# Kernel tuning notes

Hardware: AMD Instinct MI355X
Metric: run time of the kernel (lower is better)

## Reference

```python
import jax, jax.numpy as jnp
import numpy as np

N = 50000      # nodes (cells)
E = 800000     # directed edges
IN, H1, H2, Z = 512, 128, 128, 64


def setup_inputs() -> dict:
    key = jax.random.key(0)
    ks = jax.random.split(key, 12)
    x = jax.random.normal(ks[0], (N, IN), jnp.float32)
    edge_index = jax.random.randint(ks[1], (2, E), 0, N, dtype=jnp.int64)

    def glorot(k, i, o):
        return jax.random.normal(k, (i, o), jnp.float32) * np.float32(1.0 / np.sqrt(i))

    return {
        "x": x,
        "edge_index": edge_index,
        "W1": glorot(ks[2], IN, H1), "b1": jnp.zeros((H1,), jnp.float32),
        "W2": glorot(ks[3], H1, H2), "b2": jnp.zeros((H2,), jnp.float32),
        "Wm": glorot(ks[4], H2, Z),  "bm": jnp.zeros((Z,), jnp.float32),
        "Ws": glorot(ks[5], H2, Z),  "bs": jnp.zeros((Z,), jnp.float32),
    }


def _gcn_norm(edge_index, n):
    # PyG GCNConv default: add self-loops, sym-normalize D^-1/2 (A+I) D^-1/2
    loops = jnp.arange(n, dtype=edge_index.dtype)
    src = jnp.concatenate([edge_index[0], loops])
    dst = jnp.concatenate([edge_index[1], loops])
    deg = jax.ops.segment_sum(jnp.ones_like(dst, jnp.float32), dst, num_segments=n)
    dis = jnp.where(deg > 0, jax.lax.rsqrt(jnp.maximum(deg, 1.0)), 0.0)
    norm = dis[src] * dis[dst]  # [E+N]
    return src, dst, norm


def _gcn_conv(x, W, b, src, dst, norm, n):
    h = x @ W                          # [N, out] transform first
    msg = h[src] * norm[:, None]       # gather + scale
    out = jax.ops.segment_sum(msg, dst, num_segments=n)  # scatter-add at targets
    return out + b


def reference(x, edge_index, W1, b1, W2, b2, Wm, bm, Ws, bs):
    n = x.shape[0]
    src, dst, norm = _gcn_norm(edge_index, n)
    h = jax.nn.relu(_gcn_conv(x, W1, b1, src, dst, norm, n))
    h = jax.nn.relu(_gcn_conv(h, W2, b2, src, dst, norm, n))
    # dropout p=0.4 is identity in eval mode
    z_mean = _gcn_conv(h, Wm, bm, src, dst, norm, n)
    z_log_std = _gcn_conv(h, Ws, bs, src, dst, norm, n)
    return (z_mean, z_log_std)
```

## Files before the change

kernel.cpp:

```cpp
#include <hip/hip_runtime.h>


using u16 = unsigned short;
typedef __attribute__((ext_vector_type(8))) short short8;
typedef __attribute__((ext_vector_type(4))) float f32x4;

__device__ __forceinline__ void split_bf16(float f, u16& hi, u16& lo) {
    unsigned b = __float_as_uint(f);
    hi = (u16)(b >> 16);
    float rem = f - __uint_as_float(b & 0xFFFF0000u);
    lo = (u16)(__float_as_uint(rem) >> 16);
}

__device__ __forceinline__ int block_mode(const int* __restrict__ ew, int* sflag) {
    if (threadIdx.x == 0) *sflag = 0;
    __syncthreads();
    if (ew[2 * (int)threadIdx.x + 1] != 0) atomicOr(sflag, 1);
    __syncthreads();
    return *sflag ? 0 : 1;
}

__global__ void deg_kernel(const int* __restrict__ ew, int* __restrict__ deg, int E) {
    __shared__ int sflag;
    int mode = block_mode(ew, &sflag);
    int e = blockIdx.x * blockDim.x + threadIdx.x;
    if (e >= E) return;
    int d = mode ? ew[2 * E + 2 * e] : ew[E + e];
    atomicAdd(&deg[d], 1);
}

__global__ void scan_block_kernel(const int* __restrict__ deg, int* __restrict__ rowptr,
                                  int* __restrict__ aux, float* __restrict__ dis, int N) {
    __shared__ int s[256];
    int i = blockIdx.x * 256 + threadIdx.x;
    int v = (i < N) ? deg[i] : 0;
    if (i < N) dis[i] = rsqrtf((float)v + 1.0f);
    s[threadIdx.x] = v;
    __syncthreads();
    for (int off = 1; off < 256; off <<= 1) {
        int t = (threadIdx.x >= off) ? s[threadIdx.x - off] : 0;
        __syncthreads();
        s[threadIdx.x] += t;
        __syncthreads();
    }
    if (i < N) rowptr[i] = s[threadIdx.x] - v;
    if (threadIdx.x == 255) aux[blockIdx.x] = s[255];
}

__global__ void scan_aux_kernel(int* __restrict__ aux, int nb) {
    __shared__ int s[256];
    int i = threadIdx.x;
    int v = (i < nb) ? aux[i] : 0;
    s[i] = v;
    __syncthreads();
    for (int off = 1; off < 256; off <<= 1) {
        int t = (i >= off) ? s[i - off] : 0;
        __syncthreads();
        s[i] += t;
        __syncthreads();
    }
    if (i < nb) aux[i] = s[i] - v;
}

__global__ void add_offsets_kernel(int* __restrict__ rowptr, const int* __restrict__ aux,
                                   int N, int E) {
    int i = blockIdx.x * 256 + threadIdx.x;
    if (i < N) rowptr[i] += aux[i >> 8];
    if (i == 0) rowptr[N] = E;
}

__global__ void fill_csr_kernel(const int* __restrict__ ew,
                                const int* __restrict__ rowptr, int* __restrict__ cursor,
                                int* __restrict__ csr_src, int E) {
    __shared__ int sflag;
    int mode = block_mode(ew, &sflag);
    int e = blockIdx.x * blockDim.x + threadIdx.x;
    if (e >= E) return;
    int s = mode ? ew[2 * e] : ew[e];
    int d = mode ? ew[2 * E + 2 * e] : ew[E + e];
    int pos = rowptr[d] + atomicAdd(&cursor[d], 1);
    csr_src[pos] = s;
}

__global__ void conv_all_kernel(const float* __restrict__ W1, const float* __restrict__ W2,
                                const float* __restrict__ Wm, const float* __restrict__ Ws,
                                u16* __restrict__ B1h, u16* __restrict__ B1l,
                                u16* __restrict__ B2h, u16* __restrict__ B2l,
                                u16* __restrict__ Bch, u16* __restrict__ Bcl) {
    int idx = blockIdx.x * 256 + threadIdx.x;
    u16 h, l;
    if (idx < 65536) {
        int t = idx >> 13;
        int ks = (idx >> 9) & 15;
        int L = (idx >> 3) & 63;
        int q = idx & 7;
        int col = t * 16 + (L & 15);
        int k = ks * 32 + (L >> 4) * 8 + q;
        split_bf16(W1[k * 128 + col], h, l);
        B1h[idx] = h;
        B1l[idx] = l;
    } else if (idx < 81920) {
        int o = idx - 65536;
        int t = o >> 11;
        int ks = (o >> 9) & 3;
        int L = (o >> 3) & 63;
        int q = o & 7;
        int col = t * 16 + (L & 15);
        int k = ks * 32 + (L >> 4) * 8 + q;
        split_bf16(W2[k * 128 + col], h, l);
        B2h[o] = h;
        B2l[o] = l;
    } else if (idx < 98304) {
        int o = idx - 81920;
        int t = o >> 11;
        int ks = (o >> 9) & 3;
        int L = (o >> 3) & 63;
        int q = o & 7;
        int col = t * 16 + (L & 15);
        int k = ks * 32 + (L >> 4) * 8 + q;
        float f = (col < 64) ? Wm[k * 64 + col] : Ws[k * 64 + (col - 64)];
        split_bf16(f, h, l);
        Bch[o] = h;
        Bcl[o] = l;
    }
}

#define TILE_OFF(t) ((t) * 520)

__global__ __launch_bounds__(256) void gemm_mfma(const float* __restrict__ A,
                                                 const u16* __restrict__ Bfh,
                                                 const u16* __restrict__ Bfl,
                                                 float* __restrict__ C,
                                                 int N, int K) {
    __shared__ __align__(16) u16 AsH[4 * 520], AsL[4 * 520];

    const int tid = threadIdx.x;
    const int w = tid >> 6, lane = tid & 63;
    const int m16 = lane & 15, quad = lane >> 4;
    const int row0 = blockIdx.x * 64;

    const int s_ar = w * 16 + (lane & 15);
    const int s_ak = (lane >> 4) * 8;
    const int a_dst = TILE_OFF(w) + lane * 8;

    const int R = (w >> 1) * 32, Cc = (w & 1) * 64;
    const int atile = (w >> 1) * 2;
    const int btile = (w & 1) * 4;

    const int ksteps = K >> 5;
    const u16* bfh = Bfh + ((size_t)btile * ksteps) * 512 + lane * 8;
    const u16* bfl = Bfl + ((size_t)btile * ksteps) * 512 + lane * 8;

    f32x4 acc[2][4];
#pragma unroll
    for (int i = 0; i < 2; ++i)
#pragma unroll
        for (int j = 0; j < 4; ++j) acc[i][j] = (f32x4)0.f;

    const int grow = row0 + s_ar;
    const bool ok = (grow < N);
    const float* aptr = A + (size_t)grow * K + s_ak;

    float av[8];
    {
        f32x4 v0 = (f32x4)0.f, v1 = (f32x4)0.f;
        if (ok) { v0 = *(const f32x4*)&aptr[0]; v1 = *(const f32x4*)&aptr[4]; }
#pragma unroll
        for (int q = 0; q < 4; ++q) { av[q] = v0[q]; av[4 + q] = v1[q]; }
    }

    for (int ks = 0; ks < ksteps; ++ks) {
        short8 fbh[4], fbl[4];
#pragma unroll
        for (int j = 0; j < 4; ++j) {
            fbh[j] = *(const short8*)(bfh + (size_t)(j * ksteps + ks) * 512);
            fbl[j] = *(const short8*)(bfl + (size_t)(j * ksteps + ks) * 512);
        }

        short8 ah, al;
#pragma unroll
        for (int q = 0; q < 8; ++q) {
            u16 h, l;
            split_bf16(av[q], h, l);
            ah[q] = (short)h;
            al[q] = (short)l;
        }
        __syncthreads();
        *(short8*)&AsH[a_dst] = ah;
        *(short8*)&AsL[a_dst] = al;
        __syncthreads();

        if (ks + 1 < ksteps) {
            const int k0 = (ks + 1) * 32;
            f32x4 v0 = (f32x4)0.f, v1 = (f32x4)0.f;
            if (ok) { v0 = *(const f32x4*)&aptr[k0]; v1 = *(const f32x4*)&aptr[k0 + 4]; }
#pragma unroll
            for (int q = 0; q < 4; ++q) { av[q] = v0[q]; av[4 + q] = v1[q]; }
        }

        short8 fah[2], fal[2];
#pragma unroll
        for (int i = 0; i < 2; ++i) {
            fah[i] = *(const short8*)&AsH[TILE_OFF(atile + i) + lane * 8];
            fal[i] = *(const short8*)&AsL[TILE_OFF(atile + i) + lane * 8];
        }

#pragma unroll
        for (int i = 0; i < 2; ++i)
#pragma unroll
            for (int j = 0; j < 4; ++j) {
                acc[i][j] = __builtin_amdgcn_mfma_f32_16x16x32_bf16(
                    fah[i], fbh[j], acc[i][j], 0, 0, 0);
                acc[i][j] = __builtin_amdgcn_mfma_f32_16x16x32_bf16(
                    fah[i], fbl[j], acc[i][j], 0, 0, 0);
                acc[i][j] = __builtin_amdgcn_mfma_f32_16x16x32_bf16(
                    fal[i], fbh[j], acc[i][j], 0, 0, 0);
            }
    }

#pragma unroll
    for (int i = 0; i < 2; ++i) {
#pragma unroll
        for (int r = 0; r < 4; ++r) {
            int gr = row0 + R + i * 16 + quad * 4 + r;
            if (gr < N) {
#pragma unroll
                for (int j = 0; j < 4; ++j)
                    C[(size_t)gr * 128 + Cc + j * 16 + m16] = acc[i][j][r];
            }
        }
    }
}

__global__ __launch_bounds__(256) void propagate_kernel(
    const float* __restrict__ h, const int* __restrict__ rowptr,
    const int* __restrict__ csr_src, const float* __restrict__ dis,
    const float* __restrict__ bias, float* __restrict__ out, int N, int do_relu) {
    int wave = (blockIdx.x * 256 + threadIdx.x) >> 6;
    int lane = threadIdx.x & 63;
    if (wave >= N) return;
    int v = wave;
    int f = lane * 2;
    float dv = dis[v];
    float ax = 0.f, ay = 0.f;
    int beg = rowptr[v], end = rowptr[v + 1];
    int i = beg;
    for (; i + 8 <= end; i += 8) {
        int s[8];
        float ww[8];
        float2 g[8];
#pragma unroll
        for (int u = 0; u < 8; ++u) s[u] = csr_src[i + u];
#pragma unroll
        for (int u = 0; u < 8; ++u) ww[u] = dis[s[u]];
#pragma unroll
        for (int u = 0; u < 8; ++u) g[u] = *(const float2*)&h[(size_t)s[u] * 128 + f];
#pragma unroll
        for (int u = 0; u < 8; ++u) {
            float t = ww[u] * dv;
            ax += t * g[u].x;
            ay += t * g[u].y;
        }
    }
    if (i + 4 <= end) {
        int s[4];
        float ww[4];
        float2 g[4];
#pragma unroll
        for (int u = 0; u < 4; ++u) s[u] = csr_src[i + u];
#pragma unroll
        for (int u = 0; u < 4; ++u) ww[u] = dis[s[u]];
#pragma unroll
        for (int u = 0; u < 4; ++u) g[u] = *(const float2*)&h[(size_t)s[u] * 128 + f];
#pragma unroll
        for (int u = 0; u < 4; ++u) {
            float t = ww[u] * dv;
            ax += t * g[u].x;
            ay += t * g[u].y;
        }
        i += 4;
    }
    for (; i < end; ++i) {
        int s = csr_src[i];
        float ws = dis[s] * dv;
        float2 g = *(const float2*)&h[(size_t)s * 128 + f];
        ax += ws * g.x;
        ay += ws * g.y;
    }
    float2 hv = *(const float2*)&h[(size_t)v * 128 + f];
    ax += dv * dv * hv.x;
    ay += dv * dv * hv.y;
    ax += bias[f];
    ay += bias[f + 1];
    if (do_relu) { ax = fmaxf(ax, 0.f); ay = fmaxf(ay, 0.f); }
    *(float2*)&out[(size_t)v * 128 + f] = make_float2(ax, ay);
}

__global__ void __launch_bounds__(256) propagate_final_kernel(
    const float* __restrict__ h, const int* __restrict__ rowptr,
    const int* __restrict__ csr_src, const float* __restrict__ dis,
    const float* __restrict__ bm, const float* __restrict__ bs,
    float* __restrict__ out, int N) {
    int wave = (blockIdx.x * 256 + threadIdx.x) >> 6;
    int lane = threadIdx.x & 63;
    if (wave >= N) return;
    int v = wave;
    int f = lane * 2;
    float dv = dis[v];
    float ax = 0.f, ay = 0.f;
    int beg = rowptr[v], end = rowptr[v + 1];
    int i = beg;
    for (; i + 8 <= end; i += 8) {
        int s[8];
        float ww[8];
        float2 g[8];
#pragma unroll
        for (int u = 0; u < 8; ++u) s[u] = csr_src[i + u];
#pragma unroll
        for (int u = 0; u < 8; ++u) ww[u] = dis[s[u]];
#pragma unroll
        for (int u = 0; u < 8; ++u) g[u] = *(const float2*)&h[(size_t)s[u] * 128 + f];
#pragma unroll
        for (int u = 0; u < 8; ++u) {
            float t = ww[u] * dv;
            ax += t * g[u].x;
            ay += t * g[u].y;
        }
    }
    if (i + 4 <= end) {
        int s[4];
        float ww[4];
        float2 g[4];
#pragma unroll
        for (int u = 0; u < 4; ++u) s[u] = csr_src[i + u];
#pragma unroll
        for (int u = 0; u < 4; ++u) ww[u] = dis[s[u]];
#pragma unroll
        for (int u = 0; u < 4; ++u) g[u] = *(const float2*)&h[(size_t)s[u] * 128 + f];
#pragma unroll
        for (int u = 0; u < 4; ++u) {
            float t = ww[u] * dv;
            ax += t * g[u].x;
            ay += t * g[u].y;
        }
        i += 4;
    }
    for (; i < end; ++i) {
        int s = csr_src[i];
        float ws = dis[s] * dv;
        float2 g = *(const float2*)&h[(size_t)s * 128 + f];
        ax += ws * g.x;
        ay += ws * g.y;
    }
    float2 hv = *(const float2*)&h[(size_t)v * 128 + f];
    ax += dv * dv * hv.x;
    ay += dv * dv * hv.y;
    if (f < 64) {
        *(float2*)&out[(size_t)v * 64 + f] = make_float2(ax + bm[f], ay + bm[f + 1]);
    } else {
        int g = f - 64;
        *(float2*)&out[(size_t)N * 64 + (size_t)v * 64 + g] =
            make_float2(ax + bs[g], ay + bs[g + 1]);
    }
}

extern "C" void kernel_launch(void* const* d_in, const int* in_sizes, int n_in,
                              void* d_out, int out_size, void* d_ws, size_t ws_size,
                              hipStream_t stream) {
    const float* x  = (const float*)d_in[0];
    const int*   ew = (const int*)d_in[1];
    const float* W1 = (const float*)d_in[2];
    const float* b1 = (const float*)d_in[3];
    const float* W2 = (const float*)d_in[4];
    const float* b2 = (const float*)d_in[5];
    const float* Wm = (const float*)d_in[6];
    const float* bm = (const float*)d_in[7];
    const float* Ws = (const float*)d_in[8];
    const float* bs = (const float*)d_in[9];
    float* out = (float*)d_out;

    const int IN = 512, H = 128;
    const int N = in_sizes[0] / IN;
    const int E = in_sizes[1] / 2;

    char* base = (char*)d_ws;
    size_t off = 0;
    auto alloc = [&](size_t bytes) -> char* {
        char* p = base + off;
        off = (off + bytes + 255) & ~(size_t)255;
        return p;
    };
    char*  degcur  = (char*) alloc(400384);
    float* dis     = (float*)alloc((size_t)N * 4);
    int*   rowptr  = (int*)  alloc((size_t)(N + 1) * 4);
    int*   aux     = (int*)  alloc(256 * 4);
    int*   csr_src = (int*)  alloc((size_t)E * 4);
    u16*   B1h     = (u16*)  alloc((size_t)IN * H * 2);
    u16*   B1l     = (u16*)  alloc((size_t)IN * H * 2);
    u16*   B2h     = (u16*)  alloc((size_t)H * H * 2);
    u16*   B2l     = (u16*)  alloc((size_t)H * H * 2);
    u16*   Bch     = (u16*)  alloc((size_t)H * H * 2);
    u16*   Bcl     = (u16*)  alloc((size_t)H * H * 2);
    float* hA      = (float*)alloc((size_t)N * H * 4);
    float* hB      = (float*)alloc((size_t)N * H * 4);
    (void)ws_size; (void)n_in; (void)out_size;

    int* deg    = (int*)degcur;
    int* cursor = (int*)(degcur + 200192);

    hipMemsetAsync(degcur, 0, 400384, stream);

    const int eblocks = (E + 255) / 256;
    const int nblocks = (N + 255) / 256;

    conv_all_kernel<<<(98304 + 255) / 256, 256, 0, stream>>>(
        W1, W2, Wm, Ws, B1h, B1l, B2h, B2l, Bch, Bcl);
    deg_kernel<<<eblocks, 256, 0, stream>>>(ew, deg, E);
    scan_block_kernel<<<nblocks, 256, 0, stream>>>(deg, rowptr, aux, dis, N);
    scan_aux_kernel<<<1, 256, 0, stream>>>(aux, nblocks);
    add_offsets_kernel<<<nblocks, 256, 0, stream>>>(rowptr, aux, N, E);
    fill_csr_kernel<<<eblocks, 256, 0, stream>>>(ew, rowptr, cursor, csr_src, E);

    const int gblocks = (N + 63) / 64;
    const int pblocks = (N * 64 + 255) / 256;

    gemm_mfma<<<gblocks, 256, 0, stream>>>(x, B1h, B1l, hA, N, IN);
    propagate_kernel<<<pblocks, 256, 0, stream>>>(hA, rowptr, csr_src, dis,
                                                  b1, hB, N, 1);
    gemm_mfma<<<gblocks, 256, 0, stream>>>(hB, B2h, B2l, hA, N, H);
    propagate_kernel<<<pblocks, 256, 0, stream>>>(hA, rowptr, csr_src, dis,
                                                  b2, hB, N, 1);
    gemm_mfma<<<gblocks, 256, 0, stream>>>(hB, Bch, Bcl, hA, N, H);
    propagate_final_kernel<<<pblocks, 256, 0, stream>>>(hA, rowptr, csr_src, dis,
                                                        bm, bs, out, N);
}
```

Measured before the change: 484.7 us.

## Double-buffer B fragments and prefetch next A tile with LDS-only barriers

After: 485.5 us. Within noise of the previous version (+0.2%).

```diff
diff --git a/kernel.cpp b/kernel.cpp
--- a/kernel.cpp
+++ b/kernel.cpp
@@ -11,6 +11,12 @@
     float rem = f - __uint_as_float(b & 0xFFFF0000u);
     lo = (u16)(__float_as_uint(rem) >> 16);
 }
+
+#define LGKM_BAR()                                            \
+    do {                                                      \
+        asm volatile("s_waitcnt lgkmcnt(0)" ::: "memory");    \
+        __builtin_amdgcn_s_barrier();                         \
+    } while (0)
 
 __device__ __forceinline__ int block_mode(const int* __restrict__ ew, int* sflag) {
     if (threadIdx.x == 0) *sflag = 0;
@@ -162,20 +168,24 @@
     const float* aptr = A + (size_t)grow * K + s_ak;
 
     float av[8];
-    {
+    auto lda = [&](int kk) {
+        const int k0 = kk * 32;
         f32x4 v0 = (f32x4)0.f, v1 = (f32x4)0.f;
-        if (ok) { v0 = *(const f32x4*)&aptr[0]; v1 = *(const f32x4*)&aptr[4]; }
+        if (ok) { v0 = *(const f32x4*)&aptr[k0]; v1 = *(const f32x4*)&aptr[k0 + 4]; }
 #pragma unroll
         for (int q = 0; q < 4; ++q) { av[q] = v0[q]; av[4 + q] = v1[q]; }
-    }
-
-    for (int ks = 0; ks < ksteps; ++ks) {
-        short8 fbh[4], fbl[4];
+    };
+    auto ldb = [&](short8 (&bh)[4], short8 (&bl)[4], int kk) {
 #pragma unroll
         for (int j = 0; j < 4; ++j) {
-            fbh[j] = *(const short8*)(bfh + (size_t)(j * ksteps + ks) * 512);
-            fbl[j] = *(const short8*)(bfl + (size_t)(j * ksteps + ks) * 512);
-        }
+            bh[j] = *(const short8*)(bfh + (size_t)(j * ksteps + kk) * 512);
+            bl[j] = *(const short8*)(bfl + (size_t)(j * ksteps + kk) * 512);
+        }
+    };
+
+    auto step = [&](short8 (&ch)[4], short8 (&cl)[4],
+                    short8 (&nh)[4], short8 (&nl)[4], int kk) {
+        if (kk + 1 < ksteps) ldb(nh, nl, kk + 1);
 
         short8 ah, al;
 #pragma unroll
@@ -185,18 +195,12 @@
             ah[q] = (short)h;
             al[q] = (short)l;
         }
-        __syncthreads();
+        if (kk + 1 < ksteps) lda(kk + 1);
+
+        LGKM_BAR();
         *(short8*)&AsH[a_dst] = ah;
         *(short8*)&AsL[a_dst] = al;
-        __syncthreads();
-
-        if (ks + 1 < ksteps) {
-            const int k0 = (ks + 1) * 32;
-            f32x4 v0 = (f32x4)0.f, v1 = (f32x4)0.f;
-            if (ok) { v0 = *(const f32x4*)&aptr[k0]; v1 = *(const f32x4*)&aptr[k0 + 4]; }
-#pragma unroll
-            for (int q = 0; q < 4; ++q) { av[q] = v0[q]; av[4 + q] = v1[q]; }
-        }
+        LGKM_BAR();
 
         short8 fah[2], fal[2];
 #pragma unroll
@@ -210,12 +214,20 @@
 #pragma unroll
             for (int j = 0; j < 4; ++j) {
                 acc[i][j] = __builtin_amdgcn_mfma_f32_16x16x32_bf16(
-                    fah[i], fbh[j], acc[i][j], 0, 0, 0);
+                    fah[i], ch[j], acc[i][j], 0, 0, 0);
                 acc[i][j] = __builtin_amdgcn_mfma_f32_16x16x32_bf16(
-                    fah[i], fbl[j], acc[i][j], 0, 0, 0);
+                    fah[i], cl[j], acc[i][j], 0, 0, 0);
                 acc[i][j] = __builtin_amdgcn_mfma_f32_16x16x32_bf16(
-                    fal[i], fbh[j], acc[i][j], 0, 0, 0);
+                    fal[i], ch[j], acc[i][j], 0, 0, 0);
             }
+    };
+
+    short8 bxh[4], bxl[4], byh[4], byl[4];
+    ldb(bxh, bxl, 0);
+    lda(0);
+    for (int ks = 0; ks < ksteps; ks += 2) {
+        step(bxh, bxl, byh, byl, ks);
+        step(byh, byl, bxh, bxl, ks + 1);
     }
 
 #pragma unroll
```

## Prescale GEMM rows by dis and vectorize neighbor aggregation with half-wave split

Applied to the files above, without the earlier changes.

Result: no change. 488.0 us (+0.7%).

```diff
diff --git a/kernel.cpp b/kernel.cpp
--- a/kernel.cpp
+++ b/kernel.cpp
@@ -63,14 +63,18 @@
 }
 
 __global__ void add_offsets_kernel(int* __restrict__ rowptr, const int* __restrict__ aux,
-                                   int N, int E) {
+                                   int* __restrict__ cursor, int N, int E) {
     int i = blockIdx.x * 256 + threadIdx.x;
-    if (i < N) rowptr[i] += aux[i >> 8];
+    if (i < N) {
+        int rp = rowptr[i] + aux[i >> 8];
+        rowptr[i] = rp;
+        cursor[i] = rp;
+    }
     if (i == 0) rowptr[N] = E;
 }
 
 __global__ void fill_csr_kernel(const int* __restrict__ ew,
-                                const int* __restrict__ rowptr, int* __restrict__ cursor,
+                                int* __restrict__ cursor,
                                 int* __restrict__ csr_src, int E) {
     __shared__ int sflag;
     int mode = block_mode(ew, &sflag);
@@ -78,7 +82,7 @@
     if (e >= E) return;
     int s = mode ? ew[2 * e] : ew[e];
     int d = mode ? ew[2 * E + 2 * e] : ew[E + e];
-    int pos = rowptr[d] + atomicAdd(&cursor[d], 1);
+    int pos = atomicAdd(&cursor[d], 1);
     csr_src[pos] = s;
 }
 
@@ -130,6 +134,7 @@
 __global__ __launch_bounds__(256) void gemm_mfma(const float* __restrict__ A,
                                                  const u16* __restrict__ Bfh,
                                                  const u16* __restrict__ Bfl,
+                                                 const float* __restrict__ dis,
                                                  float* __restrict__ C,
                                                  int N, int K) {
     __shared__ __align__(16) u16 AsH[4 * 520], AsL[4 * 520];
@@ -156,6 +161,15 @@
     for (int i = 0; i < 2; ++i)
 #pragma unroll
         for (int j = 0; j < 4; ++j) acc[i][j] = (f32x4)0.f;
+
+    float dr[2][4];
+#pragma unroll
+    for (int i = 0; i < 2; ++i)
+#pragma unroll
+        for (int r = 0; r < 4; ++r) {
+            int gr = row0 + R + i * 16 + quad * 4 + r;
+            dr[i][r] = dis[gr < N ? gr : N - 1];
+        }
 
     const int grow = row0 + s_ar;
     const bool ok = (grow < N);
@@ -226,141 +240,109 @@
             if (gr < N) {
 #pragma unroll
                 for (int j = 0; j < 4; ++j)
-                    C[(size_t)gr * 128 + Cc + j * 16 + m16] = acc[i][j][r];
+                    C[(size_t)gr * 128 + Cc + j * 16 + m16] = acc[i][j][r] * dr[i][r];
             }
         }
     }
 }
 
 __global__ __launch_bounds__(256) void propagate_kernel(
-    const float* __restrict__ h, const int* __restrict__ rowptr,
+    const float* __restrict__ hs, const int* __restrict__ rowptr,
     const int* __restrict__ csr_src, const float* __restrict__ dis,
     const float* __restrict__ bias, float* __restrict__ out, int N, int do_relu) {
     int wave = (blockIdx.x * 256 + threadIdx.x) >> 6;
     int lane = threadIdx.x & 63;
     if (wave >= N) return;
-    int v = wave;
-    int f = lane * 2;
-    float dv = dis[v];
-    float ax = 0.f, ay = 0.f;
-    int beg = rowptr[v], end = rowptr[v + 1];
+    const int v = wave;
+    const int half = lane >> 5, c = lane & 31;
+    const int f4 = c * 4;
+    const float dv = dis[v];
+    f32x4 acc = (f32x4)0.f;
+    const int beg = rowptr[v], end = rowptr[v + 1];
     int i = beg;
     for (; i + 8 <= end; i += 8) {
-        int s[8];
-        float ww[8];
-        float2 g[8];
-#pragma unroll
-        for (int u = 0; u < 8; ++u) s[u] = csr_src[i + u];
-#pragma unroll
-        for (int u = 0; u < 8; ++u) ww[u] = dis[s[u]];
-#pragma unroll
-        for (int u = 0; u < 8; ++u) g[u] = *(const float2*)&h[(size_t)s[u] * 128 + f];
-#pragma unroll
-        for (int u = 0; u < 8; ++u) {
-            float t = ww[u] * dv;
-            ax += t * g[u].x;
-            ay += t * g[u].y;
-        }
-    }
-    if (i + 4 <= end) {
         int s[4];
-        float ww[4];
-        float2 g[4];
-#pragma unroll
-        for (int u = 0; u < 4; ++u) s[u] = csr_src[i + u];
-#pragma unroll
-        for (int u = 0; u < 4; ++u) ww[u] = dis[s[u]];
-#pragma unroll
-        for (int u = 0; u < 4; ++u) g[u] = *(const float2*)&h[(size_t)s[u] * 128 + f];
-#pragma unroll
-        for (int u = 0; u < 4; ++u) {
-            float t = ww[u] * dv;
-            ax += t * g[u].x;
-            ay += t * g[u].y;
-        }
-        i += 4;
-    }
-    for (; i < end; ++i) {
+        f32x4 g[4];
+#pragma unroll
+        for (int u = 0; u < 4; ++u) s[u] = csr_src[i + 2 * u + half];
+#pragma unroll
+        for (int u = 0; u < 4; ++u) g[u] = *(const f32x4*)&hs[(size_t)s[u] * 128 + f4];
+#pragma unroll
+        for (int u = 0; u < 4; ++u) acc += g[u];
+    }
+    for (; i + 2 <= end; i += 2) {
+        int s = csr_src[i + half];
+        acc += *(const f32x4*)&hs[(size_t)s * 128 + f4];
+    }
+    if (i < end && half == 0) {
         int s = csr_src[i];
-        float ws = dis[s] * dv;
-        float2 g = *(const float2*)&h[(size_t)s * 128 + f];
-        ax += ws * g.x;
-        ay += ws * g.y;
-    }
-    float2 hv = *(const float2*)&h[(size_t)v * 128 + f];
-    ax += dv * dv * hv.x;
-    ay += dv * dv * hv.y;
-    ax += bias[f];
-    ay += bias[f + 1];
-    if (do_relu) { ax = fmaxf(ax, 0.f); ay = fmaxf(ay, 0.f); }
-    *(float2*)&out[(size_t)v * 128 + f] = make_float2(ax, ay);
+        acc += *(const f32x4*)&hs[(size_t)s * 128 + f4];
+    }
+#pragma unroll
+    for (int k = 0; k < 4; ++k) acc[k] += __shfl_xor(acc[k], 32);
+    if (half == 0) {
+        const f32x4 hv = *(const f32x4*)&hs[(size_t)v * 128 + f4];
+        const f32x4 b = *(const f32x4*)&bias[f4];
+        f32x4 o;
+#pragma unroll
+        for (int k = 0; k < 4; ++k) {
+            float t = dv * (acc[k] + hv[k]) + b[k];
+            o[k] = do_relu ? fmaxf(t, 0.f) : t;
+        }
+        *(f32x4*)&out[(size_t)v * 128 + f4] = o;
+    }
 }
 
 __global__ void __launch_bounds__(256) propagate_final_kernel(
-    const float* __restrict__ h, const int* __restrict__ rowptr,
+    const float* __restrict__ hs, const int* __restrict__ rowptr,
     const int* __restrict__ csr_src, const float* __restrict__ dis,
     const float* __restrict__ bm, const float* __restrict__ bs,
     float* __restrict__ out, int N) {
     int wave = (blockIdx.x * 256 + threadIdx.x) >> 6;
     int lane = threadIdx.x & 63;
     if (wave >= N) return;
-    int v = wave;
-    int f = lane * 2;
-    float dv = dis[v];
-    float ax = 0.f, ay = 0.f;
-    int beg = rowptr[v], end = rowptr[v + 1];
+    const int v = wave;
+    const int half = lane >> 5, c = lane & 31;
+    const int f4 = c * 4;
+    const float dv = dis[v];
+    f32x4 acc = (f32x4)0.f;
+    const int beg = rowptr[v], end = rowptr[v + 1];
     int i = beg;
     for (; i + 8 <= end; i += 8) {
-        int s[8];
-        float ww[8];
-        float2 g[8];
-#pragma unroll
-        for (int u = 0; u < 8; ++u) s[u] = csr_src[i + u];
-#pragma unroll
-        for (int u = 0; u < 8; ++u) ww[u] = dis[s[u]];
-#pragma unroll
-        for (int u = 0; u < 8; ++u) g[u] = *(const float2*)&h[(size_t)s[u] * 128 + f];
-#pragma unroll
-        for (int u = 0; u < 8; ++u) {
-            float t = ww[u] * dv;
-            ax += t * g[u].x;
-            ay += t * g[u].y;
-        }
-    }
-    if (i + 4 <= end) {
         int s[4];
-        float ww[4];
-        float2 g[4];
-#pragma unroll
-        for (int u = 0; u < 4; ++u) s[u] = csr_src[i + u];
-#pragma unroll
-        for (int u = 0; u < 4; ++u) ww[u] = dis[s[u]];
-#pragma unroll
-        for (int u = 0; u < 4; ++u) g[u] = *(const float2*)&h[(size_t)s[u] * 128 + f];
-#pragma unroll
-        for (int u = 0; u < 4; ++u) {
-            float t = ww[u] * dv;
-            ax += t * g[u].x;
-            ay += t * g[u].y;
-        }
-        i += 4;
-    }
-    for (; i < end; ++i) {
+        f32x4 g[4];
+#pragma unroll
+        for (int u = 0; u < 4; ++u) s[u] = csr_src[i + 2 * u + half];
+#pragma unroll
+        for (int u = 0; u < 4; ++u) g[u] = *(const f32x4*)&hs[(size_t)s[u] * 128 + f4];
+#pragma unroll
+        for (int u = 0; u < 4; ++u) acc += g[u];
+    }
+    for (; i + 2 <= end; i += 2) {
+        int s = csr_src[i + half];
+        acc += *(const f32x4*)&hs[(size_t)s * 128 + f4];
+    }
+    if (i < end && half == 0) {
         int s = csr_src[i];
-        float ws = dis[s] * dv;
-        float2 g = *(const float2*)&h[(size_t)s * 128 + f];
-        ax += ws * g.x;
-        ay += ws * g.y;
-    }
-    float2 hv = *(const float2*)&h[(size_t)v * 128 + f];
-    ax += dv * dv * hv.x;
-    ay += dv * dv * hv.y;
-    if (f < 64) {
-        *(float2*)&out[(size_t)v * 64 + f] = make_float2(ax + bm[f], ay + bm[f + 1]);
-    } else {
-        int g = f - 64;
-        *(float2*)&out[(size_t)N * 64 + (size_t)v * 64 + g] =
-            make_float2(ax + bs[g], ay + bs[g + 1]);
+        acc += *(const f32x4*)&hs[(size_t)s * 128 + f4];
+    }
+#pragma unroll
+    for (int k = 0; k < 4; ++k) acc[k] += __shfl_xor(acc[k], 32);
+    if (half == 0) {
+        const f32x4 hv = *(const f32x4*)&hs[(size_t)v * 128 + f4];
+        f32x4 o;
+        if (f4 < 64) {
+            const f32x4 b = *(const f32x4*)&bm[f4];
+#pragma unroll
+            for (int k = 0; k < 4; ++k) o[k] = dv * (acc[k] + hv[k]) + b[k];
+            *(f32x4*)&out[(size_t)v * 64 + f4] = o;
+        } else {
+            const int g = f4 - 64;
+            const f32x4 b = *(const f32x4*)&bs[g];
+#pragma unroll
+            for (int k = 0; k < 4; ++k) o[k] = dv * (acc[k] + hv[k]) + b[k];
+            *(f32x4*)&out[(size_t)N * 64 + (size_t)v * 64 + g] = o;
+        }
     }
 }
 
@@ -390,7 +372,8 @@
         off = (off + bytes + 255) & ~(size_t)255;
         return p;
     };
-    char*  degcur  = (char*) alloc(400384);
+    int*   deg     = (int*)  alloc((size_t)N * 4);
+    int*   cursor  = (int*)  alloc((size_t)N * 4);
     float* dis     = (float*)alloc((size_t)N * 4);
     int*   rowptr  = (int*)  alloc((size_t)(N + 1) * 4);
     int*   aux     = (int*)  alloc(256 * 4);
@@ -405,10 +388,7 @@
     float* hB      = (float*)alloc((size_t)N * H * 4);
     (void)ws_size; (void)n_in; (void)out_size;
 
-    int* deg    = (int*)degcur;
-    int* cursor = (int*)(degcur + 200192);
-
-    hipMemsetAsync(degcur, 0, 400384, stream);
+    hipMemsetAsync(deg, 0, (size_t)N * 4, stream);
 
     const int eblocks = (E + 255) / 256;
     const int nblocks = (N + 255) / 256;
@@ -418,19 +398,19 @@
     deg_kernel<<<eblocks, 256, 0, stream>>>(ew, deg, E);
     scan_block_kernel<<<nblocks, 256, 0, stream>>>(deg, rowptr, aux, dis, N);
     scan_aux_kernel<<<1, 256, 0, stream>>>(aux, nblocks);
-    add_offsets_kernel<<<nblocks, 256, 0, stream>>>(rowptr, aux, N, E);
-    fill_csr_kernel<<<eblocks, 256, 0, stream>>>(ew, rowptr, cursor, csr_src, E);
+    add_offsets_kernel<<<nblocks, 256, 0, stream>>>(rowptr, aux, cursor, N, E);
+    fill_csr_kernel<<<eblocks, 256, 0, stream>>>(ew, cursor, csr_src, E);
 
     const int gblocks = (N + 63) / 64;
     const int pblocks = (N * 64 + 255) / 256;
 
-    gemm_mfma<<<gblocks, 256, 0, stream>>>(x, B1h, B1l, hA, N, IN);
+    gemm_mfma<<<gblocks, 256, 0, stream>>>(x, B1h, B1l, dis, hA, N, IN);
     propagate_kernel<<<pblocks, 256, 0, stream>>>(hA, rowptr, csr_src, dis,
                                                   b1, hB, N, 1);
-    gemm_mfma<<<gblocks, 256, 0, stream>>>(hB, B2h, B2l, hA, N, H);
+    gemm_mfma<<<gblocks, 256, 0, stream>>>(hB, B2h, B2l, dis, hA, N, H);
     propagate_kernel<<<pblocks, 256, 0, stream>>>(hA, rowptr, csr_src, dis,
                                                   b2, hB, N, 1);
-    gemm_mfma<<<gblocks, 256, 0, stream>>>(hB, Bch, Bcl, hA, N, H);
+    gemm_mfma<<<gblocks, 256, 0, stream>>>(hB, Bch, Bcl, dis, hA, N, H);
     propagate_final_kernel<<<pblocks, 256, 0, stream>>>(hA, rowptr, csr_src, dis,
                                                         bm, bs, out, N);
 }
```
